# Optimization experiments

Hardware: AMD Instinct MI355X
Metric: run time of the kernel (lower is better)

The kernel has to match this reference:

```python
import jax, jax.numpy as jnp
import numpy as np

B, N, D, H = 4, 16384, 64, 8
MIN_FREQ = 1.0 / 64.0
SCALE = 1.0
EPS = 1e-5


def layernorm(x):
    # LayerNorm over last (head-feature) dim, no affine, biased variance (torch default)
    m = jnp.mean(x, axis=-1, keepdims=True)
    v = jnp.mean(jnp.square(x - m), axis=-1, keepdims=True)
    return (x - m) * jax.lax.rsqrt(v + EPS)


def rope_freqs(pos):
    # pos: [b, n, 1] 1-D coordinates -> freqs [b, n, D]
    inv_freq = 1.0 / (10000.0 ** (jnp.arange(0, D, 2, dtype=jnp.float32) / D))  # [D/2]
    t = pos[..., 0] * (SCALE / MIN_FREQ)                                         # [b, n]
    f = t[..., None] * inv_freq                                                  # [b, n, D/2]
    return jnp.concatenate([f, f], axis=-1)                                      # [b, n, D]


def rotate_half(x):
    x1, x2 = jnp.split(x, 2, axis=-1)
    return jnp.concatenate([-x2, x1], axis=-1)


def apply_rope(x, freqs):
    # x: [b, h, n, d], freqs: [b, n, d]
    c = jnp.cos(freqs)[:, None]
    s = jnp.sin(freqs)[:, None]
    return x * c + rotate_half(x) * s


def setup_inputs() -> dict:
    key = jax.random.key(0)
    ks = jax.random.split(key, 6)
    gain = 1.0 / D
    return {
        "x": jax.random.normal(ks[0], (B, N, D), dtype=jnp.float32),
        "pos": jax.random.uniform(ks[1], (B, N, 1), dtype=jnp.float32),
        "Wq": jax.random.normal(ks[2], (D, D * H), dtype=jnp.float32) * gain,
        "Wk": jax.random.normal(ks[3], (D, D * H), dtype=jnp.float32) * gain,
        "Wv": jax.random.normal(ks[4], (D, D * H), dtype=jnp.float32) * gain,
        "Wo": jax.random.normal(ks[5], (D * H, D), dtype=jnp.float32) * gain,
    }


def reference(x, pos, Wq, Wk, Wv, Wo):
    b, n, _ = x.shape

    def proj(W):
        # [b, n, d] @ [d, h*d] -> [b, h, n, d]
        y = jnp.einsum("bnd,de->bne", x, W)
        return y.reshape(b, n, H, D).transpose(0, 2, 1, 3)

    q, k, v = proj(Wq), proj(Wk), proj(Wv)

    # galerkin: layernorm k and v (no mask path)
    k = layernorm(k)
    v = layernorm(v)

    # RoPE on q, k
    freqs = rope_freqs(pos)
    q = apply_rope(q, freqs)
    k = apply_rope(k, freqs)

    # linear attention: z = q @ (k^T v) / n
    kv = jnp.einsum("bhnd,bhne->bhde", k, v)          # [b, h, d, d]
    z = jnp.einsum("bhnd,bhde->bhne", q, kv) / n      # [b, h, n, d]
    z = z.transpose(0, 2, 1, 3).reshape(b, n, H * D)  # [b, n, h*d]

    return jnp.einsum("bne,ed->bnd", z, Wo)           # out_proj (dropout=0)
```

## Files before the change

### kernel.cpp

```cpp
#include <hip/hip_runtime.h>

#define B_ 4
#define N_ 16384
#define D_ 64
#define H_ 8
#define E_ 512
#define NCHUNK 24
#define NTILES (N_ / 64)

typedef __attribute__((ext_vector_type(8))) short short8;
typedef __attribute__((ext_vector_type(4))) float f32x4;

__device__ __forceinline__ unsigned short f2b(float f) {
    unsigned u = __float_as_uint(f);
    return (unsigned short)((u + 0x7fffu + ((u >> 16) & 1u)) >> 16);
}

template<int CTRL>
__device__ __forceinline__ float dppadd(float x) {
    int y = __builtin_amdgcn_update_dpp(0, __float_as_int(x), CTRL, 0xF, 0xF, true);
    return x + __int_as_float(y);
}
__device__ __forceinline__ float rowsum16(float x) {
    x = dppadd<0xB1>(x);
    x = dppadd<0x4E>(x);
    x = dppadd<0x141>(x);
    x = dppadd<0x140>(x);
    return x;
}

__global__ __launch_bounds__(256) void k_init(float* kv_sum)
{
    kv_sum[blockIdx.x * 256 + threadIdx.x] = 0.f;
}

__global__ __launch_bounds__(256) void k_pack(
    const float* __restrict__ Wq, const float* __restrict__ Wk,
    const float* __restrict__ Wv,
    unsigned short* __restrict__ WqB, unsigned short* __restrict__ WkB,
    unsigned short* __restrict__ WvB)
{
    const float* src = (blockIdx.y == 0) ? Wq : (blockIdx.y == 1) ? Wk : Wv;
    unsigned short* dst = (blockIdx.y == 0) ? WqB : (blockIdx.y == 1) ? WkB : WvB;
    int id = blockIdx.x * 256 + threadIdx.x;
    int kin = id >> 9, f = id & 511;
    int h = f >> 6, feat = f & 63;
    int nt = feat >> 4, cc = feat & 15;
    int half = kin >> 5, qd = (kin >> 3) & 3, e = kin & 7;
    dst[(size_t)h * 4096 + (((nt * 2 + half) * 64 + qd * 16 + cc) * 8) + e]
        = f2b(src[id]);
}

__global__ __launch_bounds__(256) void k_xp(const float* __restrict__ x,
                                            unsigned short* __restrict__ xblob)
{
    int idx = blockIdx.x * 256 + threadIdx.x;
    int lane = idx & 63, fr = (idx >> 6) & 1, tb = (idx >> 7) & 1023, b = idx >> 17;
    int cc = lane & 15, qd = lane >> 4;
    const float* src = &x[((size_t)b * N_ + tb * 16 + cc) * 64 + fr * 32 + qd * 8];
    float4 v0 = *(const float4*)src;
    float4 v1 = *(const float4*)(src + 4);
    ushort4 u0, u1;
    u0.x = f2b(v0.x); u0.y = f2b(v0.y); u0.z = f2b(v0.z); u0.w = f2b(v0.w);
    u1.x = f2b(v1.x); u1.y = f2b(v1.y); u1.z = f2b(v1.z); u1.w = f2b(v1.w);
    *(ushort4*)&xblob[(size_t)idx * 8]     = u0;
    *(ushort4*)&xblob[(size_t)idx * 8 + 4] = u1;
}

__global__ __launch_bounds__(256, 3) void k_kv(
    const unsigned short* __restrict__ xblob,
    const float* __restrict__ pos,
    const unsigned short* __restrict__ WkB,
    const unsigned short* __restrict__ WvB,
    float* __restrict__ kv_sum)
{
    const int b = blockIdx.z, h = blockIdx.y, chunk = blockIdx.x;
    const int tid  = threadIdx.x;
    const int lane = tid & 63;
    const int w    = tid >> 6;
    const int c    = lane & 15;
    const int quad = lane >> 4;
    const int m0   = w * 16;

    __shared__ unsigned short kbuf[64 * 72];
    __shared__ unsigned short vbuf[64 * 72];

    short8 WK[8], WV[8];
    {
        const unsigned short* wk0 = WkB + (size_t)h * 4096 + (size_t)lane * 8;
        const unsigned short* wv0 = WvB + (size_t)h * 4096 + (size_t)lane * 8;
        #pragma unroll
        for (int fr = 0; fr < 8; ++fr) WK[fr] = *(const short8*)&wk0[fr * 512];
        #pragma unroll
        for (int fr = 0; fr < 8; ++fr) WV[fr] = *(const short8*)&wv0[fr * 512];
    }

    const float invf_lo = exp2f(-0.4152410118609203f * (float)c);
    const float invf_hi = invf_lo * 0.01f;

    f32x4 akv[4];
    #pragma unroll
    for (int nt = 0; nt < 4; ++nt) akv[nt] = (f32x4){0.f, 0.f, 0.f, 0.f};

    short8 a0, a1;
    float tp[4];
    {
        int tb = chunk * 4 + w;
        const unsigned short* xb = xblob + (size_t)((b * 1024 + tb) * 2) * 512 + lane * 8;
        a0 = *(const short8*)&xb[0];
        a1 = *(const short8*)&xb[512];
        #pragma unroll
        for (int r = 0; r < 4; ++r)
            tp[r] = pos[(size_t)b * N_ + chunk * 64 + m0 + quad * 4 + r] * 64.0f;
    }

    for (int tile = chunk; tile < NTILES; tile += NCHUNK) {
        f32x4 ak[4], av[4];
        #pragma unroll
        for (int nt = 0; nt < 4; ++nt) {
            f32x4 z = {0.f, 0.f, 0.f, 0.f};
            z = __builtin_amdgcn_mfma_f32_16x16x32_bf16(a0, WK[nt * 2 + 0], z, 0, 0, 0);
            ak[nt] = __builtin_amdgcn_mfma_f32_16x16x32_bf16(a1, WK[nt * 2 + 1], z, 0, 0, 0);
            f32x4 y = {0.f, 0.f, 0.f, 0.f};
            y = __builtin_amdgcn_mfma_f32_16x16x32_bf16(a0, WV[nt * 2 + 0], y, 0, 0, 0);
            av[nt] = __builtin_amdgcn_mfma_f32_16x16x32_bf16(a1, WV[nt * 2 + 1], y, 0, 0, 0);
        }

        float cl[4], sl[4], ch[4], sh[4];
        #pragma unroll
        for (int r = 0; r < 4; ++r) {
            float al = tp[r] * invf_lo, ah = tp[r] * invf_hi;
            cl[r] = __cosf(al); sl[r] = __sinf(al);
            ch[r] = __cosf(ah); sh[r] = __sinf(ah);
        }

        const int tn = tile + NCHUNK;
        if (tn < NTILES) {
            int tb = tn * 4 + w;
            const unsigned short* xb = xblob + (size_t)((b * 1024 + tb) * 2) * 512 + lane * 8;
            a0 = *(const short8*)&xb[0];
            a1 = *(const short8*)&xb[512];
            #pragma unroll
            for (int r = 0; r < 4; ++r)
                tp[r] = pos[(size_t)b * N_ + tn * 64 + m0 + quad * 4 + r] * 64.0f;
        }

        #pragma unroll
        for (int r = 0; r < 4; ++r) {
            float sk  = ak[0][r] + ak[1][r] + ak[2][r] + ak[3][r];
            float sk2 = ak[0][r]*ak[0][r] + ak[1][r]*ak[1][r] + ak[2][r]*ak[2][r] + ak[3][r]*ak[3][r];
            float sv  = av[0][r] + av[1][r] + av[2][r] + av[3][r];
            float sv2 = av[0][r]*av[0][r] + av[1][r]*av[1][r] + av[2][r]*av[2][r] + av[3][r]*av[3][r];
            sk = rowsum16(sk); sk2 = rowsum16(sk2);
            sv = rowsum16(sv); sv2 = rowsum16(sv2);
            float mk = sk * (1.0f / 64.0f);
            float rk = rsqrtf(sk2 * (1.0f / 64.0f) - mk * mk + 1e-5f);
            float mv = sv * (1.0f / 64.0f);
            float rv = rsqrtf(sv2 * (1.0f / 64.0f) - mv * mv + 1e-5f);
            #pragma unroll
            for (int nt = 0; nt < 4; ++nt) {
                ak[nt][r] = (ak[nt][r] - mk) * rk;
                av[nt][r] = (av[nt][r] - mv) * rv;
            }
        }

        #pragma unroll
        for (int r = 0; r < 4; ++r) {
            float lo0 = ak[0][r], hi0 = ak[2][r];
            ak[0][r] = lo0 * cl[r] - hi0 * sl[r];
            ak[2][r] = hi0 * cl[r] + lo0 * sl[r];
            float lo1 = ak[1][r], hi1 = ak[3][r];
            ak[1][r] = lo1 * ch[r] - hi1 * sh[r];
            ak[3][r] = hi1 * ch[r] + lo1 * sh[r];
        }

        __syncthreads();

        #pragma unroll
        for (int nt = 0; nt < 4; ++nt) {
            ushort4 pk, pv;
            pk.x = f2b(ak[nt][0]); pk.y = f2b(ak[nt][1]); pk.z = f2b(ak[nt][2]); pk.w = f2b(ak[nt][3]);
            pv.x = f2b(av[nt][0]); pv.y = f2b(av[nt][1]); pv.z = f2b(av[nt][2]); pv.w = f2b(av[nt][3]);
            *(ushort4*)&kbuf[(nt * 16 + c) * 72 + m0 + quad * 4] = pk;
            *(ushort4*)&vbuf[(nt * 16 + c) * 72 + m0 + quad * 4] = pv;
        }
        __syncthreads();

        short8 ka0 = *(const short8*)&kbuf[(m0 + c) * 72 + quad * 8];
        short8 ka1 = *(const short8*)&kbuf[(m0 + c) * 72 + 32 + quad * 8];
        #pragma unroll
        for (int nt = 0; nt < 4; ++nt) {
            short8 vb0 = *(const short8*)&vbuf[(nt * 16 + c) * 72 + quad * 8];
            short8 vb1 = *(const short8*)&vbuf[(nt * 16 + c) * 72 + 32 + quad * 8];
            akv[nt] = __builtin_amdgcn_mfma_f32_16x16x32_bf16(ka0, vb0, akv[nt], 0, 0, 0);
            akv[nt] = __builtin_amdgcn_mfma_f32_16x16x32_bf16(ka1, vb1, akv[nt], 0, 0, 0);
        }
    }

    float* dst = kv_sum + (size_t)(b * H_ + h) * 4096;
    #pragma unroll
    for (int nt = 0; nt < 4; ++nt)
        #pragma unroll
        for (int r = 0; r < 4; ++r)
            atomicAdd(&dst[(size_t)(16 * w + quad * 4 + r) * 64 + nt * 16 + c], akv[nt][r]);
}

__global__ __launch_bounds__(256) void k_m(
    const float* __restrict__ kv_sum,
    const float* __restrict__ Wo,
    unsigned short* __restrict__ MTB)
{
    const int h = blockIdx.x, b = blockIdx.y;
    const int tid = threadIdx.x;
    __shared__ float kvs[64 * 65];
    __shared__ float wos[64 * 68];

    for (int i = tid; i < 4096; i += 256) {
        int d = i >> 6, e = i & 63;
        kvs[d * 65 + e] = kv_sum[(size_t)(b * H_ + h) * 4096 + i];
    }
    for (int i = tid; i < 1024; i += 256) {
        int dp = i >> 4, j4 = (i & 15) * 4;
        *(float4*)&wos[dp * 68 + j4] = *(const float4*)&Wo[(size_t)(h * 64 + dp) * 64 + j4];
    }
    __syncthreads();

    const int j0 = (tid & 15) * 4, d0 = (tid >> 4) * 4;
    float acc[4][4] = {{0.f}};
    #pragma unroll 4
    for (int dp = 0; dp < 64; ++dp) {
        float a_[4];
        #pragma unroll
        for (int i = 0; i < 4; ++i) a_[i] = kvs[(d0 + i) * 65 + dp];
        float4 w4 = *(const float4*)&wos[dp * 68 + j0];
        float w_[4] = {w4.x, w4.y, w4.z, w4.w};
        #pragma unroll
        for (int i = 0; i < 4; ++i)
            #pragma unroll
            for (int j = 0; j < 4; ++j)
                acc[i][j] += a_[i] * w_[j];
    }
    const float inv_n = 1.0f / (float)N_;
    unsigned short* dst = MTB + (size_t)(b * H_ + h) * 4096;
    #pragma unroll
    for (int i = 0; i < 4; ++i)
        #pragma unroll
        for (int j = 0; j < 4; ++j) {
            int d = d0 + i, jj = j0 + j;
            int nt = jj >> 4, cc = jj & 15;
            int half = d >> 5, qd = (d >> 3) & 3, e = d & 7;
            dst[(((nt * 2 + half) * 64 + qd * 16 + cc) * 8) + e] = f2b(acc[i][j] * inv_n);
        }
}

__global__ __launch_bounds__(256, 3) void k_out(
    const unsigned short* __restrict__ xblob,
    const float* __restrict__ pos,
    const unsigned short* __restrict__ WqB,
    const unsigned short* __restrict__ MTB,
    float* __restrict__ out)
{
    const int b = blockIdx.y;
    const int n0 = blockIdx.x * 64;
    const int tid  = threadIdx.x;
    const int lane = tid & 63;
    const int w    = tid >> 6;
    const int c    = lane & 15;
    const int quad = lane >> 4;
    const int m0   = w * 16;

    __shared__ unsigned short qbuf[64 * 72];

    const int tb = blockIdx.x * 4 + w;
    const unsigned short* xb = xblob + (size_t)((b * 1024 + tb) * 2) * 512 + lane * 8;
    short8 a0 = *(const short8*)&xb[0];
    short8 a1 = *(const short8*)&xb[512];

    const unsigned short* wq0 = WqB + (size_t)lane * 8;
    const unsigned short* mt0 = MTB + (size_t)(b * H_) * 4096 + (size_t)lane * 8;
    short8 W[8], Mt[8];
    #pragma unroll
    for (int fr = 0; fr < 8; ++fr) W[fr]  = *(const short8*)&wq0[fr * 512];
    #pragma unroll
    for (int fr = 0; fr < 8; ++fr) Mt[fr] = *(const short8*)&mt0[fr * 512];

    const float invf_lo = exp2f(-0.4152410118609203f * (float)c);
    const float invf_hi = invf_lo * 0.01f;
    float csl[4], snl[4], csh[4], snh[4];
    #pragma unroll
    for (int r = 0; r < 4; ++r) {
        float tpv = pos[(size_t)b * N_ + n0 + m0 + quad * 4 + r] * 64.0f;
        float al = tpv * invf_lo, ah = tpv * invf_hi;
        csl[r] = __cosf(al); snl[r] = __sinf(al);
        csh[r] = __cosf(ah); snh[r] = __sinf(ah);
    }

    f32x4 oacc[4];
    #pragma unroll
    for (int nt = 0; nt < 4; ++nt) oacc[nt] = (f32x4){0.f, 0.f, 0.f, 0.f};

    #pragma unroll
    for (int h = 0; h < H_; ++h) {
        f32x4 aq[4];
        #pragma unroll
        for (int nt = 0; nt < 4; ++nt) {
            f32x4 z = {0.f, 0.f, 0.f, 0.f};
            z = __builtin_amdgcn_mfma_f32_16x16x32_bf16(a0, W[nt * 2 + 0], z, 0, 0, 0);
            aq[nt] = __builtin_amdgcn_mfma_f32_16x16x32_bf16(a1, W[nt * 2 + 1], z, 0, 0, 0);
        }

        if (h < H_ - 1) {
            #pragma unroll
            for (int fr = 0; fr < 8; ++fr)
                W[fr] = *(const short8*)&wq0[(size_t)(h + 1) * 4096 + fr * 512];
        }

        #pragma unroll
        for (int r = 0; r < 4; ++r) {
            float lo0 = aq[0][r], hi0 = aq[2][r];
            aq[0][r] = lo0 * csl[r] - hi0 * snl[r];
            aq[2][r] = hi0 * csl[r] + lo0 * snl[r];
            float lo1 = aq[1][r], hi1 = aq[3][r];
            aq[1][r] = lo1 * csh[r] - hi1 * snh[r];
            aq[3][r] = hi1 * csh[r] + lo1 * snh[r];
        }

        #pragma unroll
        for (int nt = 0; nt < 4; ++nt)
            #pragma unroll
            for (int r = 0; r < 4; ++r)
                qbuf[(m0 + quad * 4 + r) * 72 + nt * 16 + c] = f2b(aq[nt][r]);

        short8 qa0 = *(const short8*)&qbuf[(m0 + c) * 72 + quad * 8];
        short8 qa1 = *(const short8*)&qbuf[(m0 + c) * 72 + 32 + quad * 8];
        #pragma unroll
        for (int nt = 0; nt < 4; ++nt) {
            oacc[nt] = __builtin_amdgcn_mfma_f32_16x16x32_bf16(qa0, Mt[nt * 2 + 0], oacc[nt], 0, 0, 0);
            oacc[nt] = __builtin_amdgcn_mfma_f32_16x16x32_bf16(qa1, Mt[nt * 2 + 1], oacc[nt], 0, 0, 0);
        }

        if (h < H_ - 1) {
            #pragma unroll
            for (int fr = 0; fr < 8; ++fr)
                Mt[fr] = *(const short8*)&mt0[(size_t)(h + 1) * 4096 + fr * 512];
        }
    }

    #pragma unroll
    for (int nt = 0; nt < 4; ++nt)
        #pragma unroll
        for (int r = 0; r < 4; ++r)
            out[(size_t)(b * N_ + n0 + m0 + quad * 4 + r) * 64 + nt * 16 + c] = oacc[nt][r];
}

extern "C" void kernel_launch(void* const* d_in, const int* in_sizes, int n_in,
                              void* d_out, int out_size, void* d_ws, size_t ws_size,
                              hipStream_t stream)
{
    const float* x   = (const float*)d_in[0];
    const float* pos = (const float*)d_in[1];
    const float* Wq  = (const float*)d_in[2];
    const float* Wk  = (const float*)d_in[3];
    const float* Wv  = (const float*)d_in[4];
    const float* Wo  = (const float*)d_in[5];
    float* out = (float*)d_out;

    char* ws = (char*)d_ws;
    float* kv_sum        = (float*)ws;
    unsigned short* MTB  = (unsigned short*)(ws + 524288);
    unsigned short* WqB  = (unsigned short*)(ws + 786432);
    unsigned short* WkB  = (unsigned short*)(ws + 851968);
    unsigned short* WvB  = (unsigned short*)(ws + 917504);
    unsigned short* xblob = (unsigned short*)(ws + 983040);

    k_init<<<dim3(512), 256, 0, stream>>>(kv_sum);
    k_pack<<<dim3(128, 3), 256, 0, stream>>>(Wq, Wk, Wv, WqB, WkB, WvB);
    k_xp  <<<dim3(2048), 256, 0, stream>>>(x, xblob);
    k_kv  <<<dim3(NCHUNK, H_, B_), 256, 0, stream>>>(xblob, pos, WkB, WvB, kv_sum);
    k_m   <<<dim3(H_, B_), 256, 0, stream>>>(kv_sum, Wo, MTB);
    k_out <<<dim3(NTILES, B_), 256, 0, stream>>>(xblob, pos, WqB, MTB, out);
}
```

Measured before the change: 166.8 us.

## Merge prep kernels, double-buffer kv LDS, use packed bf16 converts, raise occupancy

Folds the zero-init, weight-pack and x-pack launches into one k_prep kernel to save launch overhead. In k_kv the K/V LDS buffers are double-buffered so one of the two barriers per tile can go, and NCHUNK rises from 24 to 32 so more blocks are in flight. Packed v_cvt_pk_bf16_f32 instructions replace the manual bf16 rounding in k_kv and k_out. Launch bounds move to 4 waves per SIMD, which could force register spills in exchange for higher occupancy.

```diff
diff --git a/kernel.cpp b/kernel.cpp
--- a/kernel.cpp
+++ b/kernel.cpp
@@ -5,15 +5,22 @@
 #define D_ 64
 #define H_ 8
 #define E_ 512
-#define NCHUNK 24
+#define NCHUNK 32
 #define NTILES (N_ / 64)
 
 typedef __attribute__((ext_vector_type(8))) short short8;
 typedef __attribute__((ext_vector_type(4))) float f32x4;
+typedef __attribute__((ext_vector_type(2))) unsigned int uint32x2;
 
 __device__ __forceinline__ unsigned short f2b(float f) {
     unsigned u = __float_as_uint(f);
     return (unsigned short)((u + 0x7fffu + ((u >> 16) & 1u)) >> 16);
+}
+
+__device__ __forceinline__ unsigned cvtpk(float a, float b) {
+    unsigned r;
+    asm("v_cvt_pk_bf16_f32 %0, %1, %2" : "=v"(r) : "v"(a), "v"(b));
+    return r;
 }
 
 template<int CTRL>
@@ -29,32 +36,35 @@
     return x;
 }
 
-__global__ __launch_bounds__(256) void k_init(float* kv_sum)
-{
-    kv_sum[blockIdx.x * 256 + threadIdx.x] = 0.f;
-}
-
-__global__ __launch_bounds__(256) void k_pack(
+__global__ __launch_bounds__(256) void k_prep(
+    const float* __restrict__ x,
     const float* __restrict__ Wq, const float* __restrict__ Wk,
     const float* __restrict__ Wv,
+    float* __restrict__ kv_sum,
     unsigned short* __restrict__ WqB, unsigned short* __restrict__ WkB,
-    unsigned short* __restrict__ WvB)
-{
-    const float* src = (blockIdx.y == 0) ? Wq : (blockIdx.y == 1) ? Wk : Wv;
-    unsigned short* dst = (blockIdx.y == 0) ? WqB : (blockIdx.y == 1) ? WkB : WvB;
-    int id = blockIdx.x * 256 + threadIdx.x;
-    int kin = id >> 9, f = id & 511;
-    int h = f >> 6, feat = f & 63;
-    int nt = feat >> 4, cc = feat & 15;
-    int half = kin >> 5, qd = (kin >> 3) & 3, e = kin & 7;
-    dst[(size_t)h * 4096 + (((nt * 2 + half) * 64 + qd * 16 + cc) * 8) + e]
-        = f2b(src[id]);
-}
-
-__global__ __launch_bounds__(256) void k_xp(const float* __restrict__ x,
-                                            unsigned short* __restrict__ xblob)
-{
-    int idx = blockIdx.x * 256 + threadIdx.x;
+    unsigned short* __restrict__ WvB,
+    unsigned short* __restrict__ xblob)
+{
+    const int bid = blockIdx.x, tid = threadIdx.x;
+    if (bid < 512) {
+        kv_sum[bid * 256 + tid] = 0.f;
+        return;
+    }
+    if (bid < 896) {
+        int i = bid - 512;
+        int mat = i >> 7, sub = i & 127;
+        const float* src = (mat == 0) ? Wq : (mat == 1) ? Wk : Wv;
+        unsigned short* dst = (mat == 0) ? WqB : (mat == 1) ? WkB : WvB;
+        int id = sub * 256 + tid;
+        int kin = id >> 9, f = id & 511;
+        int h = f >> 6, feat = f & 63;
+        int nt = feat >> 4, cc = feat & 15;
+        int half = kin >> 5, qd = (kin >> 3) & 3, e = kin & 7;
+        dst[(size_t)h * 4096 + (((nt * 2 + half) * 64 + qd * 16 + cc) * 8) + e]
+            = f2b(src[id]);
+        return;
+    }
+    int idx = (bid - 896) * 256 + tid;
     int lane = idx & 63, fr = (idx >> 6) & 1, tb = (idx >> 7) & 1023, b = idx >> 17;
     int cc = lane & 15, qd = lane >> 4;
     const float* src = &x[((size_t)b * N_ + tb * 16 + cc) * 64 + fr * 32 + qd * 8];
@@ -67,7 +77,7 @@
     *(ushort4*)&xblob[(size_t)idx * 8 + 4] = u1;
 }
 
-__global__ __launch_bounds__(256, 3) void k_kv(
+__global__ __launch_bounds__(256, 4) void k_kv(
     const unsigned short* __restrict__ xblob,
     const float* __restrict__ pos,
     const unsigned short* __restrict__ WkB,
@@ -82,8 +92,8 @@
     const int quad = lane >> 4;
     const int m0   = w * 16;
 
-    __shared__ unsigned short kbuf[64 * 72];
-    __shared__ unsigned short vbuf[64 * 72];
+    __shared__ unsigned short kbuf[2][64 * 72];
+    __shared__ unsigned short vbuf[2][64 * 72];
 
     short8 WK[8], WV[8];
     {
@@ -114,6 +124,7 @@
             tp[r] = pos[(size_t)b * N_ + chunk * 64 + m0 + quad * 4 + r] * 64.0f;
     }
 
+    int p = 0;
     for (int tile = chunk; tile < NTILES; tile += NCHUNK) {
         f32x4 ak[4], av[4];
         #pragma unroll
@@ -174,27 +185,28 @@
             ak[3][r] = hi1 * ch[r] + lo1 * sh[r];
         }
 
+        #pragma unroll
+        for (int nt = 0; nt < 4; ++nt) {
+            uint32x2 kk, vv;
+            kk[0] = cvtpk(ak[nt][0], ak[nt][1]);
+            kk[1] = cvtpk(ak[nt][2], ak[nt][3]);
+            vv[0] = cvtpk(av[nt][0], av[nt][1]);
+            vv[1] = cvtpk(av[nt][2], av[nt][3]);
+            *(uint32x2*)&kbuf[p][(nt * 16 + c) * 72 + m0 + quad * 4] = kk;
+            *(uint32x2*)&vbuf[p][(nt * 16 + c) * 72 + m0 + quad * 4] = vv;
+        }
         __syncthreads();
 
-        #pragma unroll
-        for (int nt = 0; nt < 4; ++nt) {
-            ushort4 pk, pv;
-            pk.x = f2b(ak[nt][0]); pk.y = f2b(ak[nt][1]); pk.z = f2b(ak[nt][2]); pk.w = f2b(ak[nt][3]);
-            pv.x = f2b(av[nt][0]); pv.y = f2b(av[nt][1]); pv.z = f2b(av[nt][2]); pv.w = f2b(av[nt][3]);
-            *(ushort4*)&kbuf[(nt * 16 + c) * 72 + m0 + quad * 4] = pk;
-            *(ushort4*)&vbuf[(nt * 16 + c) * 72 + m0 + quad * 4] = pv;
-        }
-        __syncthreads();
-
-        short8 ka0 = *(const short8*)&kbuf[(m0 + c) * 72 + quad * 8];
-        short8 ka1 = *(const short8*)&kbuf[(m0 + c) * 72 + 32 + quad * 8];
-        #pragma unroll
-        for (int nt = 0; nt < 4; ++nt) {
-            short8 vb0 = *(const short8*)&vbuf[(nt * 16 + c) * 72 + quad * 8];
-            short8 vb1 = *(const short8*)&vbuf[(nt * 16 + c) * 72 + 32 + quad * 8];
+        short8 ka0 = *(const short8*)&kbuf[p][(m0 + c) * 72 + quad * 8];
+        short8 ka1 = *(const short8*)&kbuf[p][(m0 + c) * 72 + 32 + quad * 8];
+        #pragma unroll
+        for (int nt = 0; nt < 4; ++nt) {
+            short8 vb0 = *(const short8*)&vbuf[p][(nt * 16 + c) * 72 + quad * 8];
+            short8 vb1 = *(const short8*)&vbuf[p][(nt * 16 + c) * 72 + 32 + quad * 8];
             akv[nt] = __builtin_amdgcn_mfma_f32_16x16x32_bf16(ka0, vb0, akv[nt], 0, 0, 0);
             akv[nt] = __builtin_amdgcn_mfma_f32_16x16x32_bf16(ka1, vb1, akv[nt], 0, 0, 0);
         }
+        p ^= 1;
     }
 
     float* dst = kv_sum + (size_t)(b * H_ + h) * 4096;
@@ -253,7 +265,7 @@
         }
 }
 
-__global__ __launch_bounds__(256, 3) void k_out(
+__global__ __launch_bounds__(256, 4) void k_out(
     const unsigned short* __restrict__ xblob,
     const float* __restrict__ pos,
     const unsigned short* __restrict__ WqB,
@@ -326,10 +338,15 @@
         }
 
         #pragma unroll
-        for (int nt = 0; nt < 4; ++nt)
-            #pragma unroll
-            for (int r = 0; r < 4; ++r)
-                qbuf[(m0 + quad * 4 + r) * 72 + nt * 16 + c] = f2b(aq[nt][r]);
+        for (int nt = 0; nt < 4; ++nt) {
+            unsigned q01 = cvtpk(aq[nt][0], aq[nt][1]);
+            unsigned q23 = cvtpk(aq[nt][2], aq[nt][3]);
+            int base = (m0 + quad * 4) * 72 + nt * 16 + c;
+            qbuf[base]       = (unsigned short)q01;
+            qbuf[base + 72]  = (unsigned short)(q01 >> 16);
+            qbuf[base + 144] = (unsigned short)q23;
+            qbuf[base + 216] = (unsigned short)(q23 >> 16);
+        }
 
         short8 qa0 = *(const short8*)&qbuf[(m0 + c) * 72 + quad * 8];
         short8 qa1 = *(const short8*)&qbuf[(m0 + c) * 72 + 32 + quad * 8];
@@ -366,16 +383,15 @@
     float* out = (float*)d_out;
 
     char* ws = (char*)d_ws;
-    float* kv_sum        = (float*)ws;
-    unsigned short* MTB  = (unsigned short*)(ws + 524288);
-    unsigned short* WqB  = (unsigned short*)(ws + 786432);
-    unsigned short* WkB  = (unsigned short*)(ws + 851968);
-    unsigned short* WvB  = (unsigned short*)(ws + 917504);
+    float* kv_sum         = (float*)ws;
+    unsigned short* MTB   = (unsigned short*)(ws + 524288);
+    unsigned short* WqB   = (unsigned short*)(ws + 786432);
+    unsigned short* WkB   = (unsigned short*)(ws + 851968);
+    unsigned short* WvB   = (unsigned short*)(ws + 917504);
     unsigned short* xblob = (unsigned short*)(ws + 983040);
 
-    k_init<<<dim3(512), 256, 0, stream>>>(kv_sum);
-    k_pack<<<dim3(128, 3), 256, 0, stream>>>(Wq, Wk, Wv, WqB, WkB, WvB);
-    k_xp  <<<dim3(2048), 256, 0, stream>>>(x, xblob);
+    k_prep<<<dim3(2944), 256, 0, stream>>>(x, Wq, Wk, Wv, kv_sum,
+                                           WqB, WkB, WvB, xblob);
     k_kv  <<<dim3(NCHUNK, H_, B_), 256, 0, stream>>>(xblob, pos, WkB, WvB, kv_sum);
     k_m   <<<dim3(H_, B_), 256, 0, stream>>>(kv_sum, Wo, MTB);
     k_out <<<dim3(NTILES, B_), 256, 0, stream>>>(xblob, pos, WqB, MTB, out);
```

Result: slower. 190.2 us (+14.1%).
